# Optimization experiments

Hardware: AMD Instinct MI355X
Metric: run time of the kernel (lower is better)

The kernel has to match this reference:

```python
import jax, jax.numpy as jnp
import numpy as np

N = 6144      # number of pedestrians
HID = 256     # hidden_dim
OUT = 32      # out_dim
NTOP = 4      # n nearest neighbours
EMB = OUT // NTOP  # per-neighbour embedding dim = 8


def setup_inputs() -> dict:
    key = jax.random.key(0)
    ks = jax.random.split(key, 12)
    r = lambda k, shp, s=1.0: (jax.random.normal(k, shp, dtype=jnp.float32) * s)
    return {
        "obs1": r(ks[0], (N, 2)),
        "obs2": r(ks[1], (N, 2)),
        "h": r(ks[2], (N, HID), 0.1),
        "c": r(ks[3], (N, HID), 0.1),
        "W_emb": r(ks[4], (4, EMB), 0.3),
        "b_emb": r(ks[5], (EMB,), 0.1),
        "W_ih": r(ks[6], (4 * HID, OUT), 0.1),
        "b_ih": r(ks[7], (4 * HID,), 0.1),
        "W_hh": r(ks[8], (4 * HID, HID), 0.1),
        "b_hh": r(ks[9], (4 * HID,), 0.1),
        "W_pool": r(ks[10], (OUT, HID), 0.1),
        "b_pool": r(ks[11], (OUT,), 0.1),
    }


def reference(obs1, obs2, h, c, W_emb, b_emb, W_ih, b_ih, W_hh, b_hh, W_pool, b_pool):
    n = obs2.shape[0]
    vel = obs2 - obs1                                   # [N,2]
    # rel_position[i, j] = obs2[j] - obs2[i]
    diff = obs2[None, :, :] - obs2[:, None, :]          # [N,N,2]
    dist = jnp.linalg.norm(diff, axis=-1)               # [N,N]
    # exclude self (torch code drops the diagonal before topk)
    dist = jnp.where(jnp.eye(n, dtype=bool), jnp.inf, dist)
    _, idx = jax.lax.top_k(-dist, NTOP)                 # [N,NTOP] indices of nearest
    nearest_pos = jnp.take_along_axis(diff, idx[:, :, None], axis=1)  # [N,NTOP,2]
    # rel_direction[i, j] = vel[j] - vel[i]
    nearest_vel = vel[idx] - vel[:, None, :]            # [N,NTOP,2]
    feat = jnp.concatenate([nearest_pos, nearest_vel], axis=-1)       # [N,NTOP,4]
    # Linear(4, EMB) + ReLU, then flatten neighbours -> [N, OUT]
    emb = jax.nn.relu(feat @ W_emb + b_emb).reshape(n, -1)
    # LSTMCell (PyTorch gate order: i, f, g, o)
    gates = emb @ W_ih.T + b_ih + h @ W_hh.T + b_hh     # [N,4*HID]
    gi, gf, gg, go = jnp.split(gates, 4, axis=-1)
    c_new = jax.nn.sigmoid(gf) * c + jax.nn.sigmoid(gi) * jnp.tanh(gg)
    h_new = jax.nn.sigmoid(go) * jnp.tanh(c_new)
    out = h_new @ W_pool.T + b_pool                     # [N,OUT]
    return out
```

## Files before the change

### kernel.cpp

```cpp
#include <hip/hip_runtime.h>
#include <math.h>

typedef unsigned short u16;
typedef unsigned long long u64;
typedef __attribute__((ext_vector_type(8))) short bf16x8;
typedef __attribute__((ext_vector_type(4))) float f32x4;

__device__ __forceinline__ float sigf(float x)  { return 1.0f / (1.0f + __expf(-x)); }
__device__ __forceinline__ float tanhf_(float x){ float e = __expf(2.0f * x); return 1.0f - 2.0f / (e + 1.0f); }
__device__ __forceinline__ u16 f2bf(float f) {
    unsigned x = __float_as_uint(f);
    return (u16)((x + 0x7fffu + ((x >> 16) & 1u)) >> 16);
}

#define INSU(KEY) do {                                                              \
    u64 _k = (KEY);                                                                 \
    k3 = (_k < k3) ? _k : k3;                                                       \
    { bool _c = k3 < k2; u64 _lo = _c ? k3 : k2, _hi = _c ? k2 : k3; k2 = _lo; k3 = _hi; } \
    { bool _c = k2 < k1; u64 _lo = _c ? k2 : k1, _hi = _c ? k1 : k2; k1 = _lo; k2 = _hi; } \
    { bool _c = k1 < k0; u64 _lo = _c ? k1 : k0, _hi = _c ? k0 : k1; k0 = _lo; k1 = _hi; } \
} while (0)

#define MRG4(X0,X1,X2,X3,Y0,Y1,Y2,Y3) do {                                          \
    float _q0 = fminf((X0),(Y3));                                                   \
    float _q1 = fminf((X1),(Y2));                                                   \
    float _q2 = fminf((X2),(Y1));                                                   \
    float _q3 = fminf((X3),(Y0));                                                   \
    float _l0 = fminf(_q0,_q2), _h0 = fmaxf(_q0,_q2);                               \
    float _l1 = fminf(_q1,_q3), _h1 = fmaxf(_q1,_q3);                               \
    (X0) = fminf(_l0,_l1); (X1) = fmaxf(_l0,_l1);                                   \
    (X2) = fminf(_h0,_h1); (X3) = fmaxf(_h0,_h1);                                   \
} while (0)

#define INS4(D, J) do {                                                              \
    float _d = (D); int _j = (J);                                                    \
    if (_d < bd3 || (_d == bd3 && _j < bj3)) {                                       \
        bd3 = _d; bj3 = _j;                                                          \
        if (bd3 < bd2 || (bd3 == bd2 && bj3 < bj2)) {                                \
            float _t = bd2; bd2 = bd3; bd3 = _t; int _u = bj2; bj2 = bj3; bj3 = _u; }\
        if (bd2 < bd1 || (bd2 == bd1 && bj2 < bj1)) {                                \
            float _t = bd1; bd1 = bd2; bd2 = _t; int _u = bj1; bj1 = bj2; bj2 = _u; }\
        if (bd1 < bd0 || (bd1 == bd0 && bj1 < bj0)) {                                \
            float _t = bd0; bd0 = bd1; bd1 = _t; int _u = bj0; bj0 = bj1; bj1 = _u; }\
    } } while (0)

__global__ void diag_kernel(float* out, int code, int out_size) {
    if (out_size > 0) out[0] = (float)code * 1.0e8f;
}

__device__ __forceinline__ void prep_item(
    int id, const float* Wih, const float* Whh, const float* Wp,
    u16* Wgf, u16* Wpf)
{
    if (id < 36864) {
        int gt = id / 576, rem = id - gt * 576;
        int kt = rem >> 6, ln = rem & 63;
        int g  = gt * 16 + (ln & 15);
        int k  = kt * 32 + (ln >> 4) * 8;
        u16* dst = Wgf + (size_t)id * 8;
        const float* src = (k < 32) ? (Wih + (size_t)g * 32 + k)
                                    : (Whh + (size_t)g * 256 + (k - 32));
        float4 v0 = ((const float4*)src)[0];
        float4 v1 = ((const float4*)src)[1];
        dst[0] = f2bf(v0.x); dst[1] = f2bf(v0.y); dst[2] = f2bf(v0.z); dst[3] = f2bf(v0.w);
        dst[4] = f2bf(v1.x); dst[5] = f2bf(v1.y); dst[6] = f2bf(v1.z); dst[7] = f2bf(v1.w);
    } else if (id < 37888) {
        int id2 = id - 36864;
        int pt = id2 >> 9, rem = id2 & 511;
        int kt = rem >> 6, ln = rem & 63;
        int o  = pt * 16 + (ln & 15);
        int k  = kt * 32 + (ln >> 4) * 8;
        u16* dst = Wpf + (size_t)id2 * 8;
        const float* src = Wp + (size_t)o * 256 + k;
        float4 v0 = ((const float4*)src)[0];
        float4 v1 = ((const float4*)src)[1];
        dst[0] = f2bf(v0.x); dst[1] = f2bf(v0.y); dst[2] = f2bf(v0.z); dst[3] = f2bf(v0.w);
        dst[4] = f2bf(v1.x); dst[5] = f2bf(v1.y); dst[6] = f2bf(v1.z); dst[7] = f2bf(v1.w);
    }
}

__global__ __launch_bounds__(512, 6) void knn_prep_lds_kernel(
    const float* __restrict__ obs1, const float* __restrict__ obs2,
    const float* __restrict__ Wemb, const float* __restrict__ bemb,
    const float* __restrict__ Wih,  const float* __restrict__ Whh,
    const float* __restrict__ Wp,
    u16* __restrict__ Wgf, u16* __restrict__ Wpf,
    int n, int knn_blocks, float* __restrict__ out)
{
    extern __shared__ __align__(16) char smem[];
    float4* s4 = (float4*)smem;
    float2* sP = (float2*)smem;

    const int t = threadIdx.x;

    if (blockIdx.x >= knn_blocks) {
        int id = (blockIdx.x - knn_blocks) * 512 + t;
        prep_item(id, Wih, Whh, Wp, Wgf, Wpf);
        return;
    }

    const float FINF = __int_as_float(0x7f800000);
    const float2* o2 = (const float2*)obs2;
    const float4* o4 = (const float4*)obs2;
    const int n2 = n >> 1;

    for (int idx = t; idx < n2; idx += 512) s4[idx] = o4[idx];
    if ((n & 1) && t == 0) sP[n - 1] = o2[n - 1];
    __syncthreads();

    const int lane = t & 63;
    const int wv   = t >> 6;
    const int i    = blockIdx.x * 8 + wv;
    if (i >= n) return;

    const float2 pi = o2[i];

    float mm0 = FINF, mm1 = FINF, mm2 = FINF, mm3 = FINF;

    int f = lane;
    for (; f + 64 < n2; f += 128) {
        float4 pa = s4[f], pb = s4[f + 64];
        int j0 = 2 * f;
        float dxa = pa.x - pi.x, dya = pa.y - pi.y;
        float da = __fadd_rn(__fmul_rn(dxa, dxa), __fmul_rn(dya, dya));
        da = (j0 == i) ? FINF : da;
        float dxb = pa.z - pi.x, dyb = pa.w - pi.y;
        float db = __fadd_rn(__fmul_rn(dxb, dxb), __fmul_rn(dyb, dyb));
        db = (j0 + 1 == i) ? FINF : db;
        mm0 = fminf(mm0, da); mm1 = fminf(mm1, db);
        int j1 = 2 * (f + 64);
        float dxc = pb.x - pi.x, dyc = pb.y - pi.y;
        float dc = __fadd_rn(__fmul_rn(dxc, dxc), __fmul_rn(dyc, dyc));
        dc = (j1 == i) ? FINF : dc;
        float dxd = pb.z - pi.x, dyd = pb.w - pi.y;
        float dd = __fadd_rn(__fmul_rn(dxd, dxd), __fmul_rn(dyd, dyd));
        dd = (j1 + 1 == i) ? FINF : dd;
        mm2 = fminf(mm2, dc); mm3 = fminf(mm3, dd);
    }
    for (; f < n2; f += 64) {
        float4 pa = s4[f];
        int j0 = 2 * f;
        float dxa = pa.x - pi.x, dya = pa.y - pi.y;
        float da = __fadd_rn(__fmul_rn(dxa, dxa), __fmul_rn(dya, dya));
        da = (j0 == i) ? FINF : da;
        float dxb = pa.z - pi.x, dyb = pa.w - pi.y;
        float db = __fadd_rn(__fmul_rn(dxb, dxb), __fmul_rn(dyb, dyb));
        db = (j0 + 1 == i) ? FINF : db;
        mm0 = fminf(mm0, da); mm1 = fminf(mm1, db);
    }
    if ((n & 1) && lane == 0) {
        float2 pj = sP[n - 1];
        float dx = pj.x - pi.x, dy = pj.y - pi.y;
        float d2 = __fadd_rn(__fmul_rn(dx, dx), __fmul_rn(dy, dy));
        d2 = (n - 1 == i) ? FINF : d2;
        mm2 = fminf(mm2, d2);
    }
    const float mn = fminf(fminf(mm0, mm1), fminf(mm2, mm3));

    float A0 = mn, A1 = FINF, A2 = FINF, A3 = FINF;
    #pragma unroll
    for (int m = 1; m < 64; m <<= 1) {
        float y0 = __shfl_xor(A0, m), y1 = __shfl_xor(A1, m);
        float y2 = __shfl_xor(A2, m), y3 = __shfl_xor(A3, m);
        MRG4(A0, A1, A2, A3, y0, y1, y2, y3);
    }
    const float thr = A3;

    u64 k0 = ~0ull, k1 = ~0ull, k2 = ~0ull, k3 = ~0ull;

    f = lane;
    for (; f < n2; f += 64) {
        float4 pa = s4[f];
        const int j0 = 2 * f;
        float dxa = pa.x - pi.x, dya = pa.y - pi.y;
        float da = __fadd_rn(__fmul_rn(dxa, dxa), __fmul_rn(dya, dya));
        if (da <= thr) {
            u64 key = (((u64)__float_as_uint(da)) << 24) | (unsigned)j0;
            key = (j0 == i) ? ~0ull : key;
            INSU(key);
        }
        float dxb = pa.z - pi.x, dyb = pa.w - pi.y;
        float db = __fadd_rn(__fmul_rn(dxb, dxb), __fmul_rn(dyb, dyb));
        if (db <= thr) {
            u64 key = (((u64)__float_as_uint(db)) << 24) | (unsigned)(j0 + 1);
            key = (j0 + 1 == i) ? ~0ull : key;
            INSU(key);
        }
    }
    if ((n & 1) && lane == 0) {
        float2 pj = sP[n - 1];
        float dx = pj.x - pi.x, dy = pj.y - pi.y;
        float d2 = __fadd_rn(__fmul_rn(dx, dx), __fmul_rn(dy, dy));
        if (d2 <= thr) {
            u64 key = (((u64)__float_as_uint(d2)) << 24) | (unsigned)(n - 1);
            key = (n - 1 == i) ? ~0ull : key;
            INSU(key);
        }
    }

    #pragma unroll
    for (int m = 1; m < 64; m <<= 1) {
        u64 o0 = __shfl_xor(k0, m), o1 = __shfl_xor(k1, m);
        u64 o2_ = __shfl_xor(k2, m), o3 = __shfl_xor(k3, m);
        INSU(o0); INSU(o1); INSU(o2_); INSU(o3);
    }

    if (lane < 4) {
        u64 kq = (lane == 0) ? k0 : (lane == 1) ? k1 : (lane == 2) ? k2 : k3;
        int jn = (int)(kq & 0xFFFFFF);
        if (jn < 0 || jn >= n) jn = 0;
        float pix = pi.x, piy = pi.y;
        float pjx = obs2[2 * jn], pjy = obs2[2 * jn + 1];
        float px = pjx - pix, py = pjy - piy;
        float vix = pix - obs1[2 * i];
        float viy = piy - obs1[2 * i + 1];
        float vx = (pjx - obs1[2 * jn])     - vix;
        float vy = (pjy - obs1[2 * jn + 1]) - viy;
        float* dst = out + (size_t)i * 32 + lane * 8;
        #pragma unroll
        for (int e = 0; e < 8; e++) {
            float a = px * Wemb[e]      + py * Wemb[8 + e]
                    + vx * Wemb[16 + e] + vy * Wemb[24 + e]
                    + bemb[e];
            dst[e] = fmaxf(a, 0.0f);
        }
    }
}

__global__ __launch_bounds__(256, 4) void knn_prep_kernel(
    const float* __restrict__ obs1, const float* __restrict__ obs2,
    const float* __restrict__ Wemb, const float* __restrict__ bemb,
    const float* __restrict__ Wih,  const float* __restrict__ Whh,
    const float* __restrict__ Wp,
    u16* __restrict__ Wgf, u16* __restrict__ Wpf,
    int n, int knn_blocks, float* __restrict__ out)
{
    const int t = threadIdx.x;

    if (blockIdx.x >= knn_blocks) {
        int id = (blockIdx.x - knn_blocks) * 256 + t;
        prep_item(id, Wih, Whh, Wp, Wgf, Wpf);
        return;
    }

    const int lane = t & 63;
    const int wv   = t >> 6;
    const int i    = blockIdx.x * 4 + wv;
    if (i >= n) return;

    const float FINF = __int_as_float(0x7f800000);
    const float2* o2 = (const float2*)obs2;
    const float4* o4 = (const float4*)obs2;
    const int n2 = n >> 1;
    const float2 pi = o2[i];

    float mm[8];
    #pragma unroll
    for (int q = 0; q < 8; q++) mm[q] = FINF;

    int f = lane;
    for (; f + 448 < n2; f += 512) {
        float4 p[8];
        #pragma unroll
        for (int q = 0; q < 8; q++) p[q] = o4[f + q * 64];
        #pragma unroll
        for (int q = 0; q < 8; q++) {
            const int j0 = 2 * (f + q * 64);
            float dxa = p[q].x - pi.x, dya = p[q].y - pi.y;
            float da = __fadd_rn(__fmul_rn(dxa, dxa), __fmul_rn(dya, dya));
            da = (j0 == i) ? FINF : da;
            float dxb = p[q].z - pi.x, dyb = p[q].w - pi.y;
            float db = __fadd_rn(__fmul_rn(dxb, dxb), __fmul_rn(dyb, dyb));
            db = (j0 + 1 == i) ? FINF : db;
            mm[q] = fminf(mm[q], fminf(da, db));
        }
    }
    for (; f < n2; f += 64) {
        float4 p = o4[f];
        const int j0 = 2 * f;
        float dxa = p.x - pi.x, dya = p.y - pi.y;
        float da = __fadd_rn(__fmul_rn(dxa, dxa), __fmul_rn(dya, dya));
        da = (j0 == i) ? FINF : da;
        float dxb = p.z - pi.x, dyb = p.w - pi.y;
        float db = __fadd_rn(__fmul_rn(dxb, dxb), __fmul_rn(dyb, dyb));
        db = (j0 + 1 == i) ? FINF : db;
        mm[0] = fminf(mm[0], fminf(da, db));
    }
    if ((n & 1) && lane == 0) {
        float2 pj = o2[n - 1];
        float dx = pj.x - pi.x, dy = pj.y - pi.y;
        float d2 = __fadd_rn(__fmul_rn(dx, dx), __fmul_rn(dy, dy));
        d2 = (n - 1 == i) ? FINF : d2;
        mm[1] = fminf(mm[1], d2);
    }
    const float mn = fminf(fminf(fminf(mm[0], mm[1]), fminf(mm[2], mm[3])),
                           fminf(fminf(mm[4], mm[5]), fminf(mm[6], mm[7])));

    float A0 = mn, A1 = FINF, A2 = FINF, A3 = FINF;
    #pragma unroll
    for (int m = 1; m < 64; m <<= 1) {
        float y0 = __shfl_xor(A0, m), y1 = __shfl_xor(A1, m);
        float y2 = __shfl_xor(A2, m), y3 = __shfl_xor(A3, m);
        MRG4(A0, A1, A2, A3, y0, y1, y2, y3);
    }
    const float thr = A3;

    u64 k0 = ~0ull, k1 = ~0ull, k2 = ~0ull, k3 = ~0ull;

    f = lane;
    for (; f < n2; f += 64) {
        float4 p = o4[f];
        const int j0 = 2 * f;
        float dxa = p.x - pi.x, dya = p.y - pi.y;
        float da = __fadd_rn(__fmul_rn(dxa, dxa), __fmul_rn(dya, dya));
        if (da <= thr) {
            u64 key = (((u64)__float_as_uint(da)) << 24) | (unsigned)j0;
            key = (j0 == i) ? ~0ull : key;
            INSU(key);
        }
        float dxb = p.z - pi.x, dyb = p.w - pi.y;
        float db = __fadd_rn(__fmul_rn(dxb, dxb), __fmul_rn(dyb, dyb));
        if (db <= thr) {
            u64 key = (((u64)__float_as_uint(db)) << 24) | (unsigned)(j0 + 1);
            key = (j0 + 1 == i) ? ~0ull : key;
            INSU(key);
        }
    }
    if ((n & 1) && lane == 0) {
        float2 pj = o2[n - 1];
        float dx = pj.x - pi.x, dy = pj.y - pi.y;
        float d2 = __fadd_rn(__fmul_rn(dx, dx), __fmul_rn(dy, dy));
        if (d2 <= thr) {
            u64 key = (((u64)__float_as_uint(d2)) << 24) | (unsigned)(n - 1);
            key = (n - 1 == i) ? ~0ull : key;
            INSU(key);
        }
    }

    #pragma unroll
    for (int m = 1; m < 64; m <<= 1) {
        u64 o0 = __shfl_xor(k0, m), o1 = __shfl_xor(k1, m);
        u64 o2_ = __shfl_xor(k2, m), o3 = __shfl_xor(k3, m);
        INSU(o0); INSU(o1); INSU(o2_); INSU(o3);
    }

    if (lane < 4) {
        u64 kq = (lane == 0) ? k0 : (lane == 1) ? k1 : (lane == 2) ? k2 : k3;
        int jn = (int)(kq & 0xFFFFFF);
        if (jn < 0 || jn >= n) jn = 0;
        float pix = pi.x, piy = pi.y;
        float pjx = obs2[2 * jn], pjy = obs2[2 * jn + 1];
        float px = pjx - pix, py = pjy - piy;
        float vix = pix - obs1[2 * i];
        float viy = piy - obs1[2 * i + 1];
        float vx = (pjx - obs1[2 * jn])     - vix;
        float vy = (pjy - obs1[2 * jn + 1]) - viy;
        float* dst = out + (size_t)i * 32 + lane * 8;
        #pragma unroll
        for (int e = 0; e < 8; e++) {
            float a = px * Wemb[e]      + py * Wemb[8 + e]
                    + vx * Wemb[16 + e] + vy * Wemb[24 + e]
                    + bemb[e];
            dst[e] = fmaxf(a, 0.0f);
        }
    }
}

__global__ __launch_bounds__(512) void lstm_kernel(
    const float* __restrict__ h,   const float* __restrict__ c,
    const u16*  __restrict__ Wgf,  const float* __restrict__ bih,
    const float* __restrict__ bhh,
    const u16*  __restrict__ Wpf,  const float* __restrict__ bp,
    int n, float* __restrict__ out)
{
    __shared__ __align__(16) char lds[17920];
    u16* sXb = (u16*)lds;
    u16* sHb = (u16*)(lds + 9472);

    const int t    = threadIdx.x;
    const int i0   = blockIdx.x * 12;
    const int lane = t & 63;
    const int wv   = t >> 6;
    const int fm   = lane & 15;
    const int fq   = lane >> 4;

    {
        int r = t >> 5, e = t & 31;
        int row = i0 + r;
        float v = (r < 12 && row < n) ? out[(size_t)row * 32 + e] : 0.0f;
        sXb[r * 296 + e] = f2bf(v);
    }
    #pragma unroll
    for (int f = t; f < 16 * 64; f += 512) {
        int r = f >> 6, k4 = f & 63;
        int row = i0 + r;
        float4 hv = (r < 12 && row < n) ? ((const float4*)h)[(size_t)row * 64 + k4]
                                        : make_float4(0.f, 0.f, 0.f, 0.f);
        u16* d = &sXb[r * 296 + 32 + k4 * 4];
        d[0] = f2bf(hv.x); d[1] = f2bf(hv.y); d[2] = f2bf(hv.z); d[3] = f2bf(hv.w);
    }
    __syncthreads();

    bf16x8 afr[9];
    #pragma unroll
    for (int kt = 0; kt < 9; kt++)
        afr[kt] = *(const bf16x8*)&sXb[fm * 296 + kt * 32 + fq * 8];

    #pragma unroll
    for (int ut2 = 0; ut2 < 2; ut2++) {
        const int ut = wv + ut2 * 8;
        const int u  = ut * 16 + fm;

        f32x4 acc[4];
        #pragma unroll
        for (int jg = 0; jg < 4; jg++) acc[jg] = (f32x4){0.f, 0.f, 0.f, 0.f};

        #pragma unroll
        for (int jg = 0; jg < 4; jg++) {
            const int gt = jg * 16 + ut;
            const u16* wbase = Wgf + ((size_t)gt * 9) * 512 + lane * 8;
            #pragma unroll
            for (int kt = 0; kt < 9; kt++) {
                bf16x8 bfr = *(const bf16x8*)(wbase + kt * 512);
                acc[jg] = __builtin_amdgcn_mfma_f32_16x16x32_bf16(afr[kt], bfr, acc[jg], 0, 0, 0);
            }
        }

        float b0 = bih[u]       + bhh[u];
        float b1 = bih[u + 256] + bhh[u + 256];
        float b2 = bih[u + 512] + bhh[u + 512];
        float b3 = bih[u + 768] + bhh[u + 768];

        #pragma unroll
        for (int r_ = 0; r_ < 4; r_++) {
            int rl = fq * 4 + r_;
            int row = i0 + rl;
            bool valid = (rl < 12) && (row < n);
            float cin = valid ? c[(size_t)row * 256 + u] : 0.0f;
            float gi = acc[0][r_] + b0;
            float gf = acc[1][r_] + b1;
            float gg = acc[2][r_] + b2;
            float go = acc[3][r_] + b3;
            float cn = sigf(gf) * cin + sigf(gi) * tanhf_(gg);
            float hn = sigf(go) * tanhf_(cn);
            sHb[rl * 264 + u] = valid ? f2bf(hn) : (u16)0;
        }
    }
    __syncthreads();

    if (wv < 2) {
        bf16x8 ah[8];
        #pragma unroll
        for (int kt = 0; kt < 8; kt++)
            ah[kt] = *(const bf16x8*)&sHb[fm * 264 + kt * 32 + fq * 8];
        const u16* wbase = Wpf + ((size_t)wv * 8) * 512 + lane * 8;
        f32x4 acc = {0.f, 0.f, 0.f, 0.f};
        #pragma unroll
        for (int kt = 0; kt < 8; kt++) {
            bf16x8 bfr = *(const bf16x8*)(wbase + kt * 512);
            acc = __builtin_amdgcn_mfma_f32_16x16x32_bf16(ah[kt], bfr, acc, 0, 0, 0);
        }
        float bias = bp[wv * 16 + fm];
        #pragma unroll
        for (int r_ = 0; r_ < 4; r_++) {
            int rl = fq * 4 + r_;
            int row = i0 + rl;
            if (rl < 12 && row < n) out[(size_t)row * 32 + wv * 16 + fm] = acc[r_] + bias;
        }
    }
}

__global__ __launch_bounds__(256) void nnlstm_fallback(
    const float* __restrict__ obs1, const float* __restrict__ obs2,
    const float* __restrict__ h,    const float* __restrict__ c,
    const float* __restrict__ Wemb, const float* __restrict__ bemb,
    const float* __restrict__ Wih,  const float* __restrict__ bih,
    const float* __restrict__ Whh,  const float* __restrict__ bhh,
    const float* __restrict__ Wp,   const float* __restrict__ bp,
    int n, float* __restrict__ out)
{
    __shared__ float sMd[16][64];
    __shared__ int   sMj[16][64];
    __shared__ float sX[16][292];
    __shared__ float sH[16][264];

    const int t   = threadIdx.x;
    const int sub = t & 15;
    const int ii  = t >> 4;
    const int i0  = blockIdx.x * 16;
    const int i   = i0 + ii;

    for (int v = t; v < 16 * 256; v += 256) {
        int r = v >> 8, k = v & 255;
        int row = i0 + r;
        sX[r][32 + k] = (row < n) ? h[(size_t)row * 256 + k] : 0.0f;
    }

    float bd0 = 1e30f, bd1 = 1e30f, bd2 = 1e30f, bd3 = 1e30f;
    int   bj0 = 0x7fffffff, bj1 = 0x7fffffff, bj2 = 0x7fffffff, bj3 = 0x7fffffff;

    if (i < n) {
        const float pix = obs2[2 * i];
        const float piy = obs2[2 * i + 1];
        for (int j = sub; j < n; j += 16) {
            float dx = obs2[2 * j]     - pix;
            float dy = obs2[2 * j + 1] - piy;
            float d2 = __fadd_rn(__fmul_rn(dx, dx), __fmul_rn(dy, dy));
            float dist = __fsqrt_rn(d2);
            if (j == i) continue;
            INS4(dist, j);
        }
    }
    sMd[ii][sub * 4 + 0] = bd0;  sMj[ii][sub * 4 + 0] = bj0;
    sMd[ii][sub * 4 + 1] = bd1;  sMj[ii][sub * 4 + 1] = bj1;
    sMd[ii][sub * 4 + 2] = bd2;  sMj[ii][sub * 4 + 2] = bj2;
    sMd[ii][sub * 4 + 3] = bd3;  sMj[ii][sub * 4 + 3] = bj3;
    __syncthreads();

    if (t < 16) {
        const int r = t;
        const int irow = i0 + r;
        float bd0 = 1e30f, bd1 = 1e30f, bd2 = 1e30f, bd3 = 1e30f;
        int   bj0 = 0x7fffffff, bj1 = 0x7fffffff, bj2 = 0x7fffffff, bj3 = 0x7fffffff;
        for (int q = 0; q < 64; q++) { INS4(sMd[r][q], sMj[r][q]); }

        if (irow < n) {
            float pix = obs2[2 * irow], piy = obs2[2 * irow + 1];
            float vix = pix - obs1[2 * irow];
            float viy = piy - obs1[2 * irow + 1];
            #pragma unroll
            for (int q2 = 0; q2 < 4; q2++) {
                int jn = (q2 == 0) ? bj0 : (q2 == 1) ? bj1 : (q2 == 2) ? bj2 : bj3;
                if (jn < 0 || jn >= n) jn = 0;
                float pjx = obs2[2 * jn], pjy = obs2[2 * jn + 1];
                float px = pjx - pix, py = pjy - piy;
                float vx = (pjx - obs1[2 * jn])     - vix;
                float vy = (pjy - obs1[2 * jn + 1]) - viy;
                #pragma unroll
                for (int e = 0; e < 8; e++) {
                    float a = px * Wemb[e]      + py * Wemb[8 + e]
                            + vx * Wemb[16 + e] + vy * Wemb[24 + e]
                            + bemb[e];
                    sX[r][q2 * 8 + e] = fmaxf(a, 0.0f);
                }
            }
        } else {
            for (int e = 0; e < 32; e++) sX[r][e] = 0.0f;
        }
    }
    __syncthreads();

    const int uu = t;
    float acc[4][16];
    #pragma unroll
    for (int j = 0; j < 4; j++) {
        float b = bih[uu + 256 * j] + bhh[uu + 256 * j];
        #pragma unroll
        for (int r = 0; r < 16; r++) acc[j][r] = b;
    }

    for (int kc = 0; kc < 288; kc++) {
        float w[4];
        #pragma unroll
        for (int j = 0; j < 4; j++) {
            int g = uu + 256 * j;
            w[j] = (kc < 32) ? Wih[(size_t)g * 32 + kc]
                             : Whh[(size_t)g * 256 + (kc - 32)];
        }
        #pragma unroll
        for (int r = 0; r < 16; r++) {
            float x = sX[r][kc];
            #pragma unroll
            for (int j = 0; j < 4; j++) acc[j][r] += w[j] * x;
        }
    }

    for (int r = 0; r < 16; r++) {
        int row = i0 + r;
        float cin = (row < n) ? c[(size_t)row * 256 + uu] : 0.0f;
        float cn = sigf(acc[1][r]) * cin + sigf(acc[0][r]) * tanhf(acc[2][r]);
        float hn = sigf(acc[3][r]) * tanhf(cn);
        sH[r][uu] = hn;
    }
    __syncthreads();

    for (int v = t; v < 16 * 32; v += 256) {
        int r = v >> 5, o = v & 31;
        int row = i0 + r;
        if (row >= n) continue;
        float a = bp[o];
        for (int kc = 0; kc < 256; kc++)
            a += Wp[(size_t)o * 256 + kc] * sH[r][kc];
        out[(size_t)row * 32 + o] = a;
    }
}

extern "C" void kernel_launch(void* const* d_in, const int* in_sizes, int n_in,
                              void* d_out, int out_size, void* d_ws, size_t ws_size,
                              hipStream_t stream) {
    float* out = (float*)d_out;

    int code = 0, n = 0;
    if (n_in != 12) code = 1;
    else {
        n = in_sizes[1] / 2;
        if (n <= 4 || in_sizes[1] != 2 * n)          code = 2;
        else if (in_sizes[0]  != 2 * n)              code = 3;
        else if (in_sizes[2]  != 256 * n)            code = 4;
        else if (in_sizes[3]  != 256 * n)            code = 5;
        else if (in_sizes[4]  != 32 || in_sizes[5] != 8)        code = 6;
        else if (in_sizes[6]  != 32768 || in_sizes[7] != 1024)  code = 7;
        else if (in_sizes[8]  != 262144 || in_sizes[9] != 1024) code = 8;
        else if (in_sizes[10] != 8192 || in_sizes[11] != 32)    code = 9;
        else if (out_size != 32 * n)                 code = 10;
    }
    if (code != 0) {
        diag_kernel<<<1, 1, 0, stream>>>(out, code, out_size);
        return;
    }

    const float* obs1   = (const float*)d_in[0];
    const float* obs2   = (const float*)d_in[1];
    const float* h      = (const float*)d_in[2];
    const float* c      = (const float*)d_in[3];
    const float* W_emb  = (const float*)d_in[4];
    const float* b_emb  = (const float*)d_in[5];
    const float* W_ih   = (const float*)d_in[6];
    const float* b_ih   = (const float*)d_in[7];
    const float* W_hh   = (const float*)d_in[8];
    const float* b_hh   = (const float*)d_in[9];
    const float* W_pool = (const float*)d_in[10];
    const float* b_pool = (const float*)d_in[11];

    const size_t wgf_bytes = (size_t)36864 * 8 * sizeof(u16);
    const size_t wpf_bytes = (size_t)1024 * 8 * sizeof(u16);

    if (ws_size >= wgf_bytes + wpf_bytes && n <= (1 << 24)) {
        u16* Wgf = (u16*)d_ws;
        u16* Wpf = (u16*)((char*)d_ws + wgf_bytes);
        const size_t lds_bytes = (size_t)((n + 1) & ~1) * 8;
        if (lds_bytes <= 49152) {
            int knn_blocks = (n + 7) / 8;
            int prep_blocks = (37888 + 511) / 512;
            knn_prep_lds_kernel<<<knn_blocks + prep_blocks, 512, lds_bytes, stream>>>(
                obs1, obs2, W_emb, b_emb, W_ih, W_hh, W_pool, Wgf, Wpf,
                n, knn_blocks, out);
        } else {
            int knn_blocks = (n + 3) / 4;
            knn_prep_kernel<<<knn_blocks + 148, 256, 0, stream>>>(
                obs1, obs2, W_emb, b_emb, W_ih, W_hh, W_pool, Wgf, Wpf,
                n, knn_blocks, out);
        }
        lstm_kernel<<<(n + 11) / 12, 512, 0, stream>>>(
            h, c, Wgf, b_ih, b_hh, Wpf, b_pool, n, out);
    } else {
        nnlstm_fallback<<<(n + 15) / 16, 256, 0, stream>>>(
            obs1, obs2, h, c, W_emb, b_emb, W_ih, b_ih, W_hh, b_hh,
            W_pool, b_pool, n, out);
    }
}
```

Before: 131.1 us.

## Fuse two-pass kNN threshold search into single-pass guarded top-4 insertion

Replaces the min-distance pass, wave-wide top-4 threshold merge, and second filtered pass with one pass that keeps a per-lane sorted top-4 of 64-bit keys. Each candidate is inserted only if its key beats the current fourth-best. This removes a second read of the positions from shared memory and the threshold shuffle reduction. In exchange, every candidate needs 64-bit key construction and comparison, and the insertion branch can diverge across lanes.

```diff
diff --git a/kernel.cpp b/kernel.cpp
--- a/kernel.cpp
+++ b/kernel.cpp
@@ -99,7 +99,6 @@
         return;
     }
 
-    const float FINF = __int_as_float(0x7f800000);
     const float2* o2 = (const float2*)obs2;
     const float4* o4 = (const float4*)obs2;
     const int n2 = n >> 1;
@@ -115,87 +114,67 @@
 
     const float2 pi = o2[i];
 
-    float mm0 = FINF, mm1 = FINF, mm2 = FINF, mm3 = FINF;
+    u64 k0 = ~0ull, k1 = ~0ull, k2 = ~0ull, k3 = ~0ull;
 
     int f = lane;
     for (; f + 64 < n2; f += 128) {
         float4 pa = s4[f], pb = s4[f + 64];
-        int j0 = 2 * f;
-        float dxa = pa.x - pi.x, dya = pa.y - pi.y;
-        float da = __fadd_rn(__fmul_rn(dxa, dxa), __fmul_rn(dya, dya));
-        da = (j0 == i) ? FINF : da;
-        float dxb = pa.z - pi.x, dyb = pa.w - pi.y;
-        float db = __fadd_rn(__fmul_rn(dxb, dxb), __fmul_rn(dyb, dyb));
-        db = (j0 + 1 == i) ? FINF : db;
-        mm0 = fminf(mm0, da); mm1 = fminf(mm1, db);
-        int j1 = 2 * (f + 64);
-        float dxc = pb.x - pi.x, dyc = pb.y - pi.y;
-        float dc = __fadd_rn(__fmul_rn(dxc, dxc), __fmul_rn(dyc, dyc));
-        dc = (j1 == i) ? FINF : dc;
-        float dxd = pb.z - pi.x, dyd = pb.w - pi.y;
-        float dd = __fadd_rn(__fmul_rn(dxd, dxd), __fmul_rn(dyd, dyd));
-        dd = (j1 + 1 == i) ? FINF : dd;
-        mm2 = fminf(mm2, dc); mm3 = fminf(mm3, dd);
+        const int j0 = 2 * f;
+        {
+            float dx = pa.x - pi.x, dy = pa.y - pi.y;
+            float d2 = __fadd_rn(__fmul_rn(dx, dx), __fmul_rn(dy, dy));
+            u64 key = (((u64)__float_as_uint(d2)) << 24) | (unsigned)j0;
+            key = (j0 == i) ? ~0ull : key;
+            if (key < k3) { INSU(key); }
+        }
+        {
+            float dx = pa.z - pi.x, dy = pa.w - pi.y;
+            float d2 = __fadd_rn(__fmul_rn(dx, dx), __fmul_rn(dy, dy));
+            u64 key = (((u64)__float_as_uint(d2)) << 24) | (unsigned)(j0 + 1);
+            key = (j0 + 1 == i) ? ~0ull : key;
+            if (key < k3) { INSU(key); }
+        }
+        const int j1 = 2 * (f + 64);
+        {
+            float dx = pb.x - pi.x, dy = pb.y - pi.y;
+            float d2 = __fadd_rn(__fmul_rn(dx, dx), __fmul_rn(dy, dy));
+            u64 key = (((u64)__float_as_uint(d2)) << 24) | (unsigned)j1;
+            key = (j1 == i) ? ~0ull : key;
+            if (key < k3) { INSU(key); }
+        }
+        {
+            float dx = pb.z - pi.x, dy = pb.w - pi.y;
+            float d2 = __fadd_rn(__fmul_rn(dx, dx), __fmul_rn(dy, dy));
+            u64 key = (((u64)__float_as_uint(d2)) << 24) | (unsigned)(j1 + 1);
+            key = (j1 + 1 == i) ? ~0ull : key;
+            if (key < k3) { INSU(key); }
+        }
     }
     for (; f < n2; f += 64) {
         float4 pa = s4[f];
-        int j0 = 2 * f;
-        float dxa = pa.x - pi.x, dya = pa.y - pi.y;
-        float da = __fadd_rn(__fmul_rn(dxa, dxa), __fmul_rn(dya, dya));
-        da = (j0 == i) ? FINF : da;
-        float dxb = pa.z - pi.x, dyb = pa.w - pi.y;
-        float db = __fadd_rn(__fmul_rn(dxb, dxb), __fmul_rn(dyb, dyb));
-        db = (j0 + 1 == i) ? FINF : db;
-        mm0 = fminf(mm0, da); mm1 = fminf(mm1, db);
+        const int j0 = 2 * f;
+        {
+            float dx = pa.x - pi.x, dy = pa.y - pi.y;
+            float d2 = __fadd_rn(__fmul_rn(dx, dx), __fmul_rn(dy, dy));
+            u64 key = (((u64)__float_as_uint(d2)) << 24) | (unsigned)j0;
+            key = (j0 == i) ? ~0ull : key;
+            if (key < k3) { INSU(key); }
+        }
+        {
+            float dx = pa.z - pi.x, dy = pa.w - pi.y;
+            float d2 = __fadd_rn(__fmul_rn(dx, dx), __fmul_rn(dy, dy));
+            u64 key = (((u64)__float_as_uint(d2)) << 24) | (unsigned)(j0 + 1);
+            key = (j0 + 1 == i) ? ~0ull : key;
+            if (key < k3) { INSU(key); }
+        }
     }
     if ((n & 1) && lane == 0) {
         float2 pj = sP[n - 1];
         float dx = pj.x - pi.x, dy = pj.y - pi.y;
         float d2 = __fadd_rn(__fmul_rn(dx, dx), __fmul_rn(dy, dy));
-        d2 = (n - 1 == i) ? FINF : d2;
-        mm2 = fminf(mm2, d2);
-    }
-    const float mn = fminf(fminf(mm0, mm1), fminf(mm2, mm3));
-
-    float A0 = mn, A1 = FINF, A2 = FINF, A3 = FINF;
-    #pragma unroll
-    for (int m = 1; m < 64; m <<= 1) {
-        float y0 = __shfl_xor(A0, m), y1 = __shfl_xor(A1, m);
-        float y2 = __shfl_xor(A2, m), y3 = __shfl_xor(A3, m);
-        MRG4(A0, A1, A2, A3, y0, y1, y2, y3);
-    }
-    const float thr = A3;
-
-    u64 k0 = ~0ull, k1 = ~0ull, k2 = ~0ull, k3 = ~0ull;
-
-    f = lane;
-    for (; f < n2; f += 64) {
-        float4 pa = s4[f];
-        const int j0 = 2 * f;
-        float dxa = pa.x - pi.x, dya = pa.y - pi.y;
-        float da = __fadd_rn(__fmul_rn(dxa, dxa), __fmul_rn(dya, dya));
-        if (da <= thr) {
-            u64 key = (((u64)__float_as_uint(da)) << 24) | (unsigned)j0;
-            key = (j0 == i) ? ~0ull : key;
-            INSU(key);
-        }
-        float dxb = pa.z - pi.x, dyb = pa.w - pi.y;
-        float db = __fadd_rn(__fmul_rn(dxb, dxb), __fmul_rn(dyb, dyb));
-        if (db <= thr) {
-            u64 key = (((u64)__float_as_uint(db)) << 24) | (unsigned)(j0 + 1);
-            key = (j0 + 1 == i) ? ~0ull : key;
-            INSU(key);
-        }
-    }
-    if ((n & 1) && lane == 0) {
-        float2 pj = sP[n - 1];
-        float dx = pj.x - pi.x, dy = pj.y - pi.y;
-        float d2 = __fadd_rn(__fmul_rn(dx, dx), __fmul_rn(dy, dy));
-        if (d2 <= thr) {
-            u64 key = (((u64)__float_as_uint(d2)) << 24) | (unsigned)(n - 1);
-            key = (n - 1 == i) ? ~0ull : key;
-            INSU(key);
-        }
+        u64 key = (((u64)__float_as_uint(d2)) << 24) | (unsigned)(n - 1);
+        key = (n - 1 == i) ? ~0ull : key;
+        if (key < k3) { INSU(key); }
     }
 
     #pragma unroll
```

Measured after the change: 142.3 us. 8.6% more time.

## Process 24 rows per LSTM block, reusing each weight fragment for two MFMA row tiles

Applied to the files above, without the earlier changes.

Each LSTM block now handles 24 pedestrian rows instead of 12. Every loaded gate-weight fragment feeds two MFMA row tiles, which halves the global weight traffic per row and the number of blocks. The pooling stage uses four waves to cover the two row tiles. The cost is more registers (two A-fragment sets and two accumulator sets), double the LDS, and fewer blocks (256) to spread across the GPU.

```diff
diff --git a/kernel.cpp b/kernel.cpp
--- a/kernel.cpp
+++ b/kernel.cpp
@@ -373,47 +373,51 @@
     const u16*  __restrict__ Wpf,  const float* __restrict__ bp,
     int n, float* __restrict__ out)
 {
-    __shared__ __align__(16) char lds[17920];
+    __shared__ __align__(16) char lds[35840];
     u16* sXb = (u16*)lds;
-    u16* sHb = (u16*)(lds + 9472);
+    u16* sHb = (u16*)(lds + 18944);
 
     const int t    = threadIdx.x;
-    const int i0   = blockIdx.x * 12;
+    const int i0   = blockIdx.x * 24;
     const int lane = t & 63;
     const int wv   = t >> 6;
     const int fm   = lane & 15;
     const int fq   = lane >> 4;
 
-    {
-        int r = t >> 5, e = t & 31;
+    #pragma unroll
+    for (int v = t; v < 32 * 32; v += 512) {
+        int r = v >> 5, e = v & 31;
         int row = i0 + r;
-        float v = (r < 12 && row < n) ? out[(size_t)row * 32 + e] : 0.0f;
-        sXb[r * 296 + e] = f2bf(v);
-    }
-    #pragma unroll
-    for (int f = t; f < 16 * 64; f += 512) {
+        float val = (r < 24 && row < n) ? out[(size_t)row * 32 + e] : 0.0f;
+        sXb[r * 296 + e] = f2bf(val);
+    }
+    #pragma unroll
+    for (int f = t; f < 32 * 64; f += 512) {
         int r = f >> 6, k4 = f & 63;
         int row = i0 + r;
-        float4 hv = (r < 12 && row < n) ? ((const float4*)h)[(size_t)row * 64 + k4]
+        float4 hv = (r < 24 && row < n) ? ((const float4*)h)[(size_t)row * 64 + k4]
                                         : make_float4(0.f, 0.f, 0.f, 0.f);
         u16* d = &sXb[r * 296 + 32 + k4 * 4];
         d[0] = f2bf(hv.x); d[1] = f2bf(hv.y); d[2] = f2bf(hv.z); d[3] = f2bf(hv.w);
     }
     __syncthreads();
 
-    bf16x8 afr[9];
-    #pragma unroll
-    for (int kt = 0; kt < 9; kt++)
-        afr[kt] = *(const bf16x8*)&sXb[fm * 296 + kt * 32 + fq * 8];
+    bf16x8 afr0[9], afr1[9];
+    #pragma unroll
+    for (int kt = 0; kt < 9; kt++) {
+        afr0[kt] = *(const bf16x8*)&sXb[fm * 296 + kt * 32 + fq * 8];
+        afr1[kt] = *(const bf16x8*)&sXb[(fm + 16) * 296 + kt * 32 + fq * 8];
+    }
 
     #pragma unroll
     for (int ut2 = 0; ut2 < 2; ut2++) {
         const int ut = wv + ut2 * 8;
         const int u  = ut * 16 + fm;
 
-        f32x4 acc[4];
-        #pragma unroll
-        for (int jg = 0; jg < 4; jg++) acc[jg] = (f32x4){0.f, 0.f, 0.f, 0.f};
+        f32x4 acc0[4], acc1[4];
+        #pragma unroll
+        for (int jg = 0; jg < 4; jg++) { acc0[jg] = (f32x4){0.f,0.f,0.f,0.f};
+                                         acc1[jg] = (f32x4){0.f,0.f,0.f,0.f}; }
 
         #pragma unroll
         for (int jg = 0; jg < 4; jg++) {
@@ -422,7 +426,8 @@
             #pragma unroll
             for (int kt = 0; kt < 9; kt++) {
                 bf16x8 bfr = *(const bf16x8*)(wbase + kt * 512);
-                acc[jg] = __builtin_amdgcn_mfma_f32_16x16x32_bf16(afr[kt], bfr, acc[jg], 0, 0, 0);
+                acc0[jg] = __builtin_amdgcn_mfma_f32_16x16x32_bf16(afr0[kt], bfr, acc0[jg], 0, 0, 0);
+                acc1[jg] = __builtin_amdgcn_mfma_f32_16x16x32_bf16(afr1[kt], bfr, acc1[jg], 0, 0, 0);
             }
         }
 
@@ -435,37 +440,53 @@
         for (int r_ = 0; r_ < 4; r_++) {
             int rl = fq * 4 + r_;
             int row = i0 + rl;
-            bool valid = (rl < 12) && (row < n);
+            bool valid = (row < n);
             float cin = valid ? c[(size_t)row * 256 + u] : 0.0f;
-            float gi = acc[0][r_] + b0;
-            float gf = acc[1][r_] + b1;
-            float gg = acc[2][r_] + b2;
-            float go = acc[3][r_] + b3;
+            float gi = acc0[0][r_] + b0;
+            float gf = acc0[1][r_] + b1;
+            float gg = acc0[2][r_] + b2;
+            float go = acc0[3][r_] + b3;
             float cn = sigf(gf) * cin + sigf(gi) * tanhf_(gg);
             float hn = sigf(go) * tanhf_(cn);
             sHb[rl * 264 + u] = valid ? f2bf(hn) : (u16)0;
         }
+        #pragma unroll
+        for (int r_ = 0; r_ < 4; r_++) {
+            int rl = 16 + fq * 4 + r_;
+            int row = i0 + rl;
+            bool valid = (rl < 24) && (row < n);
+            float cin = valid ? c[(size_t)row * 256 + u] : 0.0f;
+            float gi = acc1[0][r_] + b0;
+            float gf = acc1[1][r_] + b1;
+            float gg = acc1[2][r_] + b2;
+            float go = acc1[3][r_] + b3;
+            float cn = sigf(gf) * cin + sigf(gi) * tanhf_(gg);
+            float hn = sigf(go) * tanhf_(cn);
+            sHb[rl * 264 + u] = valid ? f2bf(hn) : (u16)0;
+        }
     }
     __syncthreads();
 
-    if (wv < 2) {
+    if (wv < 4) {
+        const int rt = wv >> 1;
+        const int nc = wv & 1;
         bf16x8 ah[8];
         #pragma unroll
         for (int kt = 0; kt < 8; kt++)
-            ah[kt] = *(const bf16x8*)&sHb[fm * 264 + kt * 32 + fq * 8];
-        const u16* wbase = Wpf + ((size_t)wv * 8) * 512 + lane * 8;
+            ah[kt] = *(const bf16x8*)&sHb[(fm + rt * 16) * 264 + kt * 32 + fq * 8];
+        const u16* wbase = Wpf + ((size_t)nc * 8) * 512 + lane * 8;
         f32x4 acc = {0.f, 0.f, 0.f, 0.f};
         #pragma unroll
         for (int kt = 0; kt < 8; kt++) {
             bf16x8 bfr = *(const bf16x8*)(wbase + kt * 512);
             acc = __builtin_amdgcn_mfma_f32_16x16x32_bf16(ah[kt], bfr, acc, 0, 0, 0);
         }
-        float bias = bp[wv * 16 + fm];
+        float bias = bp[nc * 16 + fm];
         #pragma unroll
         for (int r_ = 0; r_ < 4; r_++) {
-            int rl = fq * 4 + r_;
+            int rl = rt * 16 + fq * 4 + r_;
             int row = i0 + rl;
-            if (rl < 12 && row < n) out[(size_t)row * 32 + wv * 16 + fm] = acc[r_] + bias;
+            if (rl < 24 && row < n) out[(size_t)row * 32 + nc * 16 + fm] = acc[r_] + bias;
         }
     }
 }
@@ -651,7 +672,7 @@
                 obs1, obs2, W_emb, b_emb, W_ih, W_hh, W_pool, Wgf, Wpf,
                 n, knn_blocks, out);
         }
-        lstm_kernel<<<(n + 11) / 12, 512, 0, stream>>>(
+        lstm_kernel<<<(n + 23) / 24, 512, 0, stream>>>(
             h, c, Wgf, b_ih, b_hh, Wpf, b_pool, n, out);
     } else {
         nnlstm_fallback<<<(n + 15) / 16, 256, 0, stream>>>(
```

Measured after the change: 130.3 us (median of 2 runs). About the same (-0.5%).
